# Kernel tuning notes

Measured on AMD Instinct MI355X. Metric: run time of the kernel, lower is better.

## Reference

```python
import jax, jax.numpy as jnp
import numpy as np
from jax import lax

N_TOKENS = 524288
N_EXPERTS = 64
TOP_K = 8


def setup_inputs() -> dict:
    key = jax.random.key(0)
    logits = jax.random.normal(key, (N_TOKENS, N_EXPERTS), dtype=jnp.float32)
    # expert_counts / assignments / offsets are output buffers in the torch
    # module (filled by the custom kernel); pass zero placeholders.
    return {
        "expert_counts": jnp.zeros((N_EXPERTS,), dtype=jnp.int32),
        "assignments": jnp.zeros((N_TOKENS, TOP_K), dtype=jnp.int32),
        "offsets": jnp.zeros((N_TOKENS, TOP_K), dtype=jnp.int32),
        "logits": logits,
    }


def reference(expert_counts, assignments, offsets, logits):
    """Ragged top-k gating (replay_routing=False).

    Returns (expert_counts, scores, assignments, offsets, logits_out):
      scores       [N, K]  top-k softmax probabilities per token
      assignments  [N, K]  top-k expert ids per token
      offsets      [N, K]  slot of each (token, k) within its expert's
                           ragged bucket (token-major arrival order)
      expert_counts[E]     number of routed slots per expert
      logits_out           pass-through copy of logits
    """
    N, E = logits.shape
    K = assignments.shape[1]

    probs = jax.nn.softmax(logits, axis=-1)            # [N, E]
    scores, assign = lax.top_k(probs, K)               # [N, K] each
    assign = assign.astype(jnp.int32)

    flat = assign.reshape(-1)                          # [N*K], token-major
    counts = jnp.zeros((E,), jnp.int32).at[flat].add(1)

    # offsets: rank of each slot among equal-expert slots in arrival order.
    # Stable sort by expert id; within-expert rank = sorted position minus
    # the expert's segment start (exclusive cumsum of counts).
    order = jnp.argsort(flat, stable=True)             # [N*K]
    sorted_e = flat[order]
    starts = jnp.concatenate(
        [jnp.zeros((1,), jnp.int32), jnp.cumsum(counts)[:-1].astype(jnp.int32)]
    )                                                  # [E]
    ranks = jnp.arange(N * K, dtype=jnp.int32) - starts[sorted_e]
    offs = jnp.zeros((N * K,), jnp.int32).at[order].set(ranks).reshape(N, K)

    return counts, scores, assign, offs, logits
```

## Files before the change

kernel.cpp:

```cpp
#include <hip/hip_runtime.h>

#define NT 524288
#define NE 64
#define NK 8
#define TPB 128
#define NBLK (NT / TPB)
#define SPB (TPB * NK)

__global__ __launch_bounds__(256) void topk_kernel(
    const float* __restrict__ logits,
    float* __restrict__ out_scores,
    float* __restrict__ out_assign,
    float* __restrict__ out_logits,
    int* __restrict__ blockCounts)
{
    __shared__ int wcnt[4][NE];

    const int t = threadIdx.x;
    const int b = blockIdx.x;
    const int g = t & 7;
    const int tok_in_pass = t >> 3;
    const int w = t >> 6;
    const int l = t & 63;
    const unsigned long long lt_mask = (l == 0) ? 0ull : ((~0ull) >> (64 - l));

    wcnt[w][l] = 0;
    __syncthreads();

    #pragma unroll
    for (int pass = 0; pass < 4; ++pass) {
        const int ltok = pass * 32 + tok_in_pass;
        const int token = b * TPB + ltok;
        const float* lp = logits + (size_t)token * NE + g * 8;
        float4 v0 = *(const float4*)lp;
        float4 v1 = *(const float4*)(lp + 4);
        float* op = out_logits + (size_t)token * NE + g * 8;
        *(float4*)op = v0;
        *(float4*)(op + 4) = v1;

        float lv[8] = {v0.x, v0.y, v0.z, v0.w, v1.x, v1.y, v1.z, v1.w};

        float m = lv[0];
        #pragma unroll
        for (int j = 1; j < 8; ++j) m = fmaxf(m, lv[j]);
        #pragma unroll
        for (int sh = 1; sh < 8; sh <<= 1) m = fmaxf(m, __shfl_xor(m, sh, 64));

        float p[8];
        float s = 0.f;
        #pragma unroll
        for (int j = 0; j < 8; ++j) { p[j] = expf(lv[j] - m); s += p[j]; }
        #pragma unroll
        for (int sh = 1; sh < 8; sh <<= 1) s += __shfl_xor(s, sh, 64);
        const float rs = 1.0f / s;
        #pragma unroll
        for (int j = 0; j < 8; ++j) p[j] = p[j] * rs;

        float sc = 0.f; int id = 0;
        #pragma unroll
        for (int k = 0; k < NK; ++k) {
            float bv = p[0]; int bi = 0;
            #pragma unroll
            for (int j = 1; j < 8; ++j)
                if (p[j] > bv) { bv = p[j]; bi = j; }
            int bidx = g * 8 + bi;
            #pragma unroll
            for (int sh = 1; sh < 8; sh <<= 1) {
                float ov = __shfl_xor(bv, sh, 64);
                int   oi = __shfl_xor(bidx, sh, 64);
                if (ov > bv || (ov == bv && oi < bidx)) { bv = ov; bidx = oi; }
            }
            if (g == k) { sc = bv; id = bidx; }
            if ((bidx >> 3) == g) p[bidx & 7] = -1.0f;
        }

        const size_t slot = (size_t)token * NK + g;
        out_scores[slot] = sc;
        out_assign[slot] = (float)id;

        const int e = id;
        unsigned long long mask = ~0ull;
        #pragma unroll
        for (int bit = 0; bit < 6; ++bit) {
            unsigned long long bb = __ballot((e >> bit) & 1);
            mask &= ((e >> bit) & 1) ? bb : ~bb;
        }
        if ((mask & lt_mask) == 0ull)
            atomicAdd(&wcnt[w][e], __popcll(mask));
    }

    __syncthreads();
    if (t < NE) {
        const int c = wcnt[0][t] + wcnt[1][t] + wcnt[2][t] + wcnt[3][t];
        blockCounts[t * NBLK + b] = c;
    }
}

__global__ __launch_bounds__(256) void scan_kernel(
    int* __restrict__ blockCounts, float* __restrict__ out_counts)
{
    __shared__ int buf[NBLK + (NBLK >> 4)];
    __shared__ int part[256];
    const int e = blockIdx.x;
    const int t = threadIdx.x;
    int* col = blockCounts + (size_t)e * NBLK;

    #pragma unroll
    for (int i = 0; i < 16; ++i) {
        const int j = i * 256 + t;
        buf[j + (j >> 4)] = col[j];
    }
    __syncthreads();

    int loc[16];
    int s = 0;
    #pragma unroll
    for (int i = 0; i < 16; ++i) {
        const int j = t * 16 + i;
        loc[i] = s;
        s += buf[j + (j >> 4)];
    }
    part[t] = s;
    __syncthreads();

    for (int off = 1; off < 256; off <<= 1) {
        int v = (t >= off) ? part[t - off] : 0;
        __syncthreads();
        part[t] += v;
        __syncthreads();
    }
    const int run = (t == 0) ? 0 : part[t - 1];

    #pragma unroll
    for (int i = 0; i < 16; ++i) {
        const int j = t * 16 + i;
        buf[j + (j >> 4)] = run + loc[i];
    }
    __syncthreads();
    #pragma unroll
    for (int i = 0; i < 16; ++i) {
        const int j = i * 256 + t;
        col[j] = buf[j + (j >> 4)];
    }
    if (t == 255) out_counts[e] = (float)part[255];
}

__global__ __launch_bounds__(256) void offs_kernel(
    const int* __restrict__ blockCounts,
    const float* __restrict__ out_assign,
    float* __restrict__ out_offs)
{
    __shared__ int cnt[4][4][NE];
    __shared__ int base[NE];
    const int t = threadIdx.x;
    const int b = blockIdx.x;
    const int w = t >> 6;
    const int l = t & 63;
    const unsigned long long lt_mask = (l == 0) ? 0ull : ((~0ull) >> (64 - l));

    #pragma unroll
    for (int tau = 0; tau < 4; ++tau) cnt[tau][w][l] = 0;
    if (t < NE) base[t] = blockCounts[t * NBLK + b];
    __syncthreads();

    int e_r[4];
    unsigned long long mask_r[4];
    #pragma unroll
    for (int tau = 0; tau < 4; ++tau) {
        const int gslot = b * SPB + tau * 256 + t;
        const int e = (int)out_assign[gslot];
        e_r[tau] = e;
        unsigned long long mask = ~0ull;
        #pragma unroll
        for (int bit = 0; bit < 6; ++bit) {
            unsigned long long bb = __ballot((e >> bit) & 1);
            mask &= ((e >> bit) & 1) ? bb : ~bb;
        }
        mask_r[tau] = mask;
        if ((mask & lt_mask) == 0ull)
            atomicAdd(&cnt[tau][w][e], __popcll(mask));
    }
    __syncthreads();

    #pragma unroll
    for (int tau = 0; tau < 4; ++tau) {
        const int e = e_r[tau];
        int before = base[e];
        #pragma unroll
        for (int tau2 = 0; tau2 < 4; ++tau2)
            if (tau2 < tau)
                before += cnt[tau2][0][e] + cnt[tau2][1][e]
                        + cnt[tau2][2][e] + cnt[tau2][3][e];
        if (w > 0) before += cnt[tau][0][e];
        if (w > 1) before += cnt[tau][1][e];
        if (w > 2) before += cnt[tau][2][e];
        const int gslot = b * SPB + tau * 256 + t;
        out_offs[gslot] = (float)(before + __popcll(mask_r[tau] & lt_mask));
    }
}

extern "C" void kernel_launch(void* const* d_in, const int* in_sizes, int n_in,
                              void* d_out, int out_size, void* d_ws, size_t ws_size,
                              hipStream_t stream) {
    const float* logits = (const float*)d_in[3];

    float* out = (float*)d_out;
    float* out_counts = out;
    float* out_scores = out + NE;
    float* out_assign = out_scores + (size_t)NT * NK;
    float* out_offs   = out_assign + (size_t)NT * NK;
    float* out_logits = out_offs + (size_t)NT * NK;

    int* blockCounts = (int*)d_ws;

    hipLaunchKernelGGL(topk_kernel, dim3(NBLK), dim3(256), 0, stream,
                       logits, out_scores, out_assign, out_logits, blockCounts);
    hipLaunchKernelGGL(scan_kernel, dim3(NE), dim3(256), 0, stream,
                       blockCounts, out_counts);
    hipLaunchKernelGGL(offs_kernel, dim3(NBLK), dim3(256), 0, stream,
                       blockCounts, out_assign, out_offs);
}
```

Measured before the change: 328.1 us.

## Fuse top-k, scan and offsets into one cooperative persistent kernel

Replaces the three-kernel pipeline with a single cooperative kernel of 512 persistent blocks that uses grid syncs between the top-k, per-expert scan and offset phases. Each block keeps expert ids, within-wave ranks and per-pass counts in shared memory, so the offsets phase no longer re-reads out_assign from global memory and two kernel launches go away. In exchange, each block processes many more tokens serially with fewer blocks in flight, and the two grid-wide barriers add cost. The old three-kernel path remains as a fallback if the cooperative launch fails.

```diff
diff --git a/kernel.cpp b/kernel.cpp
--- a/kernel.cpp
+++ b/kernel.cpp
@@ -1,20 +1,37 @@
 #include <hip/hip_runtime.h>
+#include <hip/hip_cooperative_groups.h>
+
+namespace cg = cooperative_groups;
 
 #define NT 524288
 #define NE 64
 #define NK 8
+
+#define FB 512
+#define FTOK (NT / FB)
+#define FPASS (FTOK / 32)
+#define FSLOT (FTOK * NK)
+
 #define TPB 128
 #define NBLK (NT / TPB)
 #define SPB (TPB * NK)
 
-__global__ __launch_bounds__(256) void topk_kernel(
+__global__ __launch_bounds__(256, 2) void fused_kernel(
     const float* __restrict__ logits,
+    float* __restrict__ out_counts,
     float* __restrict__ out_scores,
     float* __restrict__ out_assign,
+    float* __restrict__ out_offs,
     float* __restrict__ out_logits,
     int* __restrict__ blockCounts)
 {
-    __shared__ int wcnt[4][NE];
+    __shared__ int cnt[FPASS][4][NE];
+    __shared__ unsigned char ids[FSLOT];
+    __shared__ unsigned char rnk[FSLOT];
+    __shared__ int base[NE];
+    __shared__ int part[256];
+
+    cg::grid_group grid = cg::this_grid();
 
     const int t = threadIdx.x;
     const int b = blockIdx.x;
@@ -24,13 +41,13 @@
     const int l = t & 63;
     const unsigned long long lt_mask = (l == 0) ? 0ull : ((~0ull) >> (64 - l));
 
-    wcnt[w][l] = 0;
-    __syncthreads();
-
-    #pragma unroll
-    for (int pass = 0; pass < 4; ++pass) {
-        const int ltok = pass * 32 + tok_in_pass;
-        const int token = b * TPB + ltok;
+    #pragma unroll
+    for (int i = 0; i < (FPASS * 4 * NE) / 256; ++i)
+        ((int*)cnt)[i * 256 + t] = 0;
+    __syncthreads();
+
+    for (int pass = 0; pass < FPASS; ++pass) {
+        const int token = b * FTOK + pass * 32 + tok_in_pass;
         const float* lp = logits + (size_t)token * NE + g * 8;
         float4 v0 = *(const float4*)lp;
         float4 v1 = *(const float4*)(lp + 4);
@@ -78,6 +95,132 @@
         out_scores[slot] = sc;
         out_assign[slot] = (float)id;
 
+        const int lslot = pass * 256 + t;
+        ids[lslot] = (unsigned char)id;
+
+        unsigned long long mask = ~0ull;
+        #pragma unroll
+        for (int bit = 0; bit < 6; ++bit) {
+            unsigned long long bb = __ballot((id >> bit) & 1);
+            mask &= ((id >> bit) & 1) ? bb : ~bb;
+        }
+        rnk[lslot] = (unsigned char)__popcll(mask & lt_mask);
+        if ((mask & lt_mask) == 0ull)
+            atomicAdd(&cnt[pass][w][id], __popcll(mask));
+    }
+    __syncthreads();
+
+    if (t < NE) {
+        int run = 0;
+        for (int i = 0; i < FPASS * 4; ++i) {
+            int* pp = &cnt[0][0][0] + i * NE + t;
+            const int v = *pp;
+            *pp = run;
+            run += v;
+        }
+        blockCounts[t * FB + b] = run;
+    }
+    grid.sync();
+
+    if (b < NE) {
+        int* col = blockCounts + b * FB;
+        int2 v = ((int2*)col)[t];
+        part[t] = v.x + v.y;
+        __syncthreads();
+        for (int off = 1; off < 256; off <<= 1) {
+            int pv = (t >= off) ? part[t - off] : 0;
+            __syncthreads();
+            part[t] += pv;
+            __syncthreads();
+        }
+        const int run = (t == 0) ? 0 : part[t - 1];
+        int2 o; o.x = run; o.y = run + v.x;
+        ((int2*)col)[t] = o;
+        if (t == 255) out_counts[b] = (float)part[255];
+    }
+    grid.sync();
+
+    if (t < NE) base[t] = blockCounts[t * FB + b];
+    __syncthreads();
+    for (int pass = 0; pass < FPASS; ++pass) {
+        const int lslot = pass * 256 + t;
+        const int e = ids[lslot];
+        const int off = base[e] + cnt[pass][w][e] + (int)rnk[lslot];
+        out_offs[(size_t)b * FSLOT + lslot] = (float)off;
+    }
+}
+
+__global__ __launch_bounds__(256) void topk_kernel(
+    const float* __restrict__ logits,
+    float* __restrict__ out_scores,
+    float* __restrict__ out_assign,
+    float* __restrict__ out_logits,
+    int* __restrict__ blockCounts)
+{
+    __shared__ int wcnt[4][NE];
+
+    const int t = threadIdx.x;
+    const int b = blockIdx.x;
+    const int g = t & 7;
+    const int tok_in_pass = t >> 3;
+    const int w = t >> 6;
+    const int l = t & 63;
+    const unsigned long long lt_mask = (l == 0) ? 0ull : ((~0ull) >> (64 - l));
+
+    wcnt[w][l] = 0;
+    __syncthreads();
+
+    #pragma unroll
+    for (int pass = 0; pass < 4; ++pass) {
+        const int ltok = pass * 32 + tok_in_pass;
+        const int token = b * TPB + ltok;
+        const float* lp = logits + (size_t)token * NE + g * 8;
+        float4 v0 = *(const float4*)lp;
+        float4 v1 = *(const float4*)(lp + 4);
+        float* op = out_logits + (size_t)token * NE + g * 8;
+        *(float4*)op = v0;
+        *(float4*)(op + 4) = v1;
+
+        float lv[8] = {v0.x, v0.y, v0.z, v0.w, v1.x, v1.y, v1.z, v1.w};
+
+        float m = lv[0];
+        #pragma unroll
+        for (int j = 1; j < 8; ++j) m = fmaxf(m, lv[j]);
+        #pragma unroll
+        for (int sh = 1; sh < 8; sh <<= 1) m = fmaxf(m, __shfl_xor(m, sh, 64));
+
+        float p[8];
+        float s = 0.f;
+        #pragma unroll
+        for (int j = 0; j < 8; ++j) { p[j] = expf(lv[j] - m); s += p[j]; }
+        #pragma unroll
+        for (int sh = 1; sh < 8; sh <<= 1) s += __shfl_xor(s, sh, 64);
+        const float rs = 1.0f / s;
+        #pragma unroll
+        for (int j = 0; j < 8; ++j) p[j] = p[j] * rs;
+
+        float sc = 0.f; int id = 0;
+        #pragma unroll
+        for (int k = 0; k < NK; ++k) {
+            float bv = p[0]; int bi = 0;
+            #pragma unroll
+            for (int j = 1; j < 8; ++j)
+                if (p[j] > bv) { bv = p[j]; bi = j; }
+            int bidx = g * 8 + bi;
+            #pragma unroll
+            for (int sh = 1; sh < 8; sh <<= 1) {
+                float ov = __shfl_xor(bv, sh, 64);
+                int   oi = __shfl_xor(bidx, sh, 64);
+                if (ov > bv || (ov == bv && oi < bidx)) { bv = ov; bidx = oi; }
+            }
+            if (g == k) { sc = bv; id = bidx; }
+            if ((bidx >> 3) == g) p[bidx & 7] = -1.0f;
+        }
+
+        const size_t slot = (size_t)token * NK + g;
+        out_scores[slot] = sc;
+        out_assign[slot] = (float)id;
+
         const int e = id;
         unsigned long long mask = ~0ull;
         #pragma unroll
@@ -103,6 +246,7 @@
     __shared__ int part[256];
     const int e = blockIdx.x;
     const int t = threadIdx.x;
+    const int PER = NBLK / 256;
     int* col = blockCounts + (size_t)e * NBLK;
 
     #pragma unroll
@@ -143,6 +287,7 @@
         col[j] = buf[j + (j >> 4)];
     }
     if (t == 255) out_counts[e] = (float)part[255];
+    (void)PER;
 }
 
 __global__ __launch_bounds__(256) void offs_kernel(
@@ -213,10 +358,21 @@
 
     int* blockCounts = (int*)d_ws;
 
-    hipLaunchKernelGGL(topk_kernel, dim3(NBLK), dim3(256), 0, stream,
-                       logits, out_scores, out_assign, out_logits, blockCounts);
-    hipLaunchKernelGGL(scan_kernel, dim3(NE), dim3(256), 0, stream,
-                       blockCounts, out_counts);
-    hipLaunchKernelGGL(offs_kernel, dim3(NBLK), dim3(256), 0, stream,
-                       blockCounts, out_assign, out_offs);
-}
+    void* args[] = {
+        (void*)&logits, (void*)&out_counts, (void*)&out_scores,
+        (void*)&out_assign, (void*)&out_offs, (void*)&out_logits,
+        (void*)&blockCounts
+    };
+    hipError_t err = hipLaunchCooperativeKernel(
+        (const void*)fused_kernel, dim3(FB), dim3(256), args, 0, stream);
+
+    if (err != hipSuccess) {
+        hipLaunchKernelGGL(topk_kernel, dim3(NBLK), dim3(256), 0, stream,
+                           logits, out_scores, out_assign, out_logits,
+                           blockCounts);
+        hipLaunchKernelGGL(scan_kernel, dim3(NE), dim3(256), 0, stream,
+                           blockCounts, out_counts);
+        hipLaunchKernelGGL(offs_kernel, dim3(NBLK), dim3(256), 0, stream,
+                           blockCounts, out_assign, out_offs);
+    }
+}
```

Result: slower. 516.4 us (+57.4%).

## Replace separate scan kernel with hierarchical super-block counts computed in finalize

Applied to the files above, without the earlier changes.

Drops the dedicated per-expert scan kernel. topk_kernel now also atomically accumulates per-expert counts into 64-block super-blocks. The finalize kernel builds each block's exclusive prefix by summing earlier super-block totals plus up to 63 earlier block counts. This removes a kernel launch and the serial scan stage, but adds a memset, global atomics, and redundant per-block prefix loops of up to about 127 strided global loads per expert thread.

```diff
diff --git a/kernel.cpp b/kernel.cpp
--- a/kernel.cpp
+++ b/kernel.cpp
@@ -6,13 +6,15 @@
 #define TPB 128
 #define NBLK (NT / TPB)
 #define SPB (TPB * NK)
+#define NSUP (NBLK / 64)
 
 __global__ __launch_bounds__(256) void topk_kernel(
     const float* __restrict__ logits,
     float* __restrict__ out_scores,
     float* __restrict__ out_assign,
     float* __restrict__ out_logits,
-    int* __restrict__ blockCounts)
+    int* __restrict__ blockCounts,
+    int* __restrict__ superCnt)
 {
     __shared__ int wcnt[4][NE];
 
@@ -29,8 +31,7 @@
 
     #pragma unroll
     for (int pass = 0; pass < 4; ++pass) {
-        const int ltok = pass * 32 + tok_in_pass;
-        const int token = b * TPB + ltok;
+        const int token = b * TPB + pass * 32 + tok_in_pass;
         const float* lp = logits + (size_t)token * NE + g * 8;
         float4 v0 = *(const float4*)lp;
         float4 v1 = *(const float4*)(lp + 4);
@@ -78,76 +79,29 @@
         out_scores[slot] = sc;
         out_assign[slot] = (float)id;
 
-        const int e = id;
         unsigned long long mask = ~0ull;
         #pragma unroll
         for (int bit = 0; bit < 6; ++bit) {
-            unsigned long long bb = __ballot((e >> bit) & 1);
-            mask &= ((e >> bit) & 1) ? bb : ~bb;
+            unsigned long long bb = __ballot((id >> bit) & 1);
+            mask &= ((id >> bit) & 1) ? bb : ~bb;
         }
         if ((mask & lt_mask) == 0ull)
-            atomicAdd(&wcnt[w][e], __popcll(mask));
+            atomicAdd(&wcnt[w][id], __popcll(mask));
     }
 
     __syncthreads();
     if (t < NE) {
         const int c = wcnt[0][t] + wcnt[1][t] + wcnt[2][t] + wcnt[3][t];
         blockCounts[t * NBLK + b] = c;
+        atomicAdd(&superCnt[t * NSUP + (b >> 6)], c);
     }
 }
 
-__global__ __launch_bounds__(256) void scan_kernel(
-    int* __restrict__ blockCounts, float* __restrict__ out_counts)
-{
-    __shared__ int buf[NBLK + (NBLK >> 4)];
-    __shared__ int part[256];
-    const int e = blockIdx.x;
-    const int t = threadIdx.x;
-    int* col = blockCounts + (size_t)e * NBLK;
-
-    #pragma unroll
-    for (int i = 0; i < 16; ++i) {
-        const int j = i * 256 + t;
-        buf[j + (j >> 4)] = col[j];
-    }
-    __syncthreads();
-
-    int loc[16];
-    int s = 0;
-    #pragma unroll
-    for (int i = 0; i < 16; ++i) {
-        const int j = t * 16 + i;
-        loc[i] = s;
-        s += buf[j + (j >> 4)];
-    }
-    part[t] = s;
-    __syncthreads();
-
-    for (int off = 1; off < 256; off <<= 1) {
-        int v = (t >= off) ? part[t - off] : 0;
-        __syncthreads();
-        part[t] += v;
-        __syncthreads();
-    }
-    const int run = (t == 0) ? 0 : part[t - 1];
-
-    #pragma unroll
-    for (int i = 0; i < 16; ++i) {
-        const int j = t * 16 + i;
-        buf[j + (j >> 4)] = run + loc[i];
-    }
-    __syncthreads();
-    #pragma unroll
-    for (int i = 0; i < 16; ++i) {
-        const int j = i * 256 + t;
-        col[j] = buf[j + (j >> 4)];
-    }
-    if (t == 255) out_counts[e] = (float)part[255];
-}
-
-__global__ __launch_bounds__(256) void offs_kernel(
+__global__ __launch_bounds__(256) void finalize_kernel(
     const int* __restrict__ blockCounts,
+    const int* __restrict__ superCnt,
     const float* __restrict__ out_assign,
+    float* __restrict__ out_counts,
     float* __restrict__ out_offs)
 {
     __shared__ int cnt[4][4][NE];
@@ -160,7 +114,21 @@
 
     #pragma unroll
     for (int tau = 0; tau < 4; ++tau) cnt[tau][w][l] = 0;
-    if (t < NE) base[t] = blockCounts[t * NBLK + b];
+
+    if (t < NE) {
+        const int s = b >> 6;
+        const int b0 = s << 6;
+        int acc = 0;
+        for (int sp = 0; sp < s; ++sp) acc += superCnt[t * NSUP + sp];
+        for (int bp = b0; bp < b; ++bp) acc += blockCounts[t * NBLK + bp];
+        base[t] = acc;
+    }
+    if (b == 0 && t < NE) {
+        int tot = 0;
+        #pragma unroll
+        for (int sp = 0; sp < NSUP; ++sp) tot += superCnt[t * NSUP + sp];
+        out_counts[t] = (float)tot;
+    }
     __syncthreads();
 
     int e_r[4];
@@ -212,11 +180,12 @@
     float* out_logits = out_offs + (size_t)NT * NK;
 
     int* blockCounts = (int*)d_ws;
+    int* superCnt    = blockCounts + (size_t)NE * NBLK;
 
+    hipMemsetAsync(superCnt, 0, (size_t)NE * NSUP * 4, stream);
     hipLaunchKernelGGL(topk_kernel, dim3(NBLK), dim3(256), 0, stream,
-                       logits, out_scores, out_assign, out_logits, blockCounts);
-    hipLaunchKernelGGL(scan_kernel, dim3(NE), dim3(256), 0, stream,
-                       blockCounts, out_counts);
-    hipLaunchKernelGGL(offs_kernel, dim3(NBLK), dim3(256), 0, stream,
-                       blockCounts, out_assign, out_offs);
+                       logits, out_scores, out_assign, out_logits,
+                       blockCounts, superCnt);
+    hipLaunchKernelGGL(finalize_kernel, dim3(NBLK), dim3(256), 0, stream,
+                       blockCounts, superCnt, out_assign, out_counts, out_offs);
 }
```

Result: slower. 350.9 us (+7.0%).
